# Kernel optimization log

Measured on AMD Instinct MI355X. Metric: run time of the kernel, lower is better.

Reference implementation:

```python
import jax, jax.numpy as jnp
import numpy as np

NUM_Q = 1000
DIM_S = 64
SIZE_M = 50
BATCH = 128
SEQ = 200


def setup_inputs() -> dict:
    key = jax.random.key(0)
    ks = jax.random.split(key, 16)
    s = 1.0 / np.sqrt(DIM_S)
    inp = {
        "q": jax.random.randint(ks[0], (BATCH, SEQ), 0, NUM_Q),
        "r": jax.random.randint(ks[1], (BATCH, SEQ), 0, 2),
        "at_s": jax.random.randint(ks[2], (BATCH, 16), 0, 30000),
        "at_m": jnp.ones((BATCH, 16), dtype=jnp.int64 if jax.config.jax_enable_x64 else jnp.int32),
        "k_emb": jax.random.normal(ks[3], (NUM_Q, DIM_S)) * s,
        "v_emb": jax.random.normal(ks[4], (2 * NUM_Q, DIM_S)) * s,
        "Mk": jax.random.normal(ks[5], (SIZE_M, DIM_S)) * s,
        "Mv0": jax.random.normal(ks[6], (SIZE_M, DIM_S)) * s,
        "We": jax.random.normal(ks[7], (DIM_S, DIM_S)) * s,
        "be": jnp.zeros((DIM_S,)),
        "Wa": jax.random.normal(ks[8], (DIM_S, DIM_S)) * s,
        "ba": jnp.zeros((DIM_S,)),
        "Wf": jax.random.normal(ks[9], (2 * DIM_S, DIM_S)) * s,
        "bf": jnp.zeros((DIM_S,)),
        "Wp": jax.random.normal(ks[10], (DIM_S, 1)) * s,
        "bp": jnp.zeros((1,)),
    }
    return inp


def reference(q, r, at_s, at_m, k_emb, v_emb, Mk, Mv0, We, be, Wa, ba, Wf, bf, Wp, bp):
    num_q = k_emb.shape[0]
    x = q + r * num_q                         # [B, n]
    k = k_emb[q]                              # [B, n, d]
    v = v_emb[x]                              # [B, n, d]
    w = jax.nn.softmax(jnp.einsum("bnd,md->bnm", k, Mk), axis=-1)  # [B, n, m]
    e = jax.nn.sigmoid(v @ We + be)           # erase gate [B, n, d]
    a = jnp.tanh(v @ Wa + ba)                 # add vector [B, n, d]

    B = q.shape[0]
    Mv_init = jnp.broadcast_to(Mv0[None], (B,) + Mv0.shape)  # [B, m, d]

    def step(Mvt, inp):
        et, at_, wt = inp                     # [B,d], [B,d], [B,m]
        Mvt = Mvt * (1.0 - wt[:, :, None] * et[:, None, :]) + wt[:, :, None] * at_[:, None, :]
        return Mvt, Mvt

    xs = (e.transpose(1, 0, 2), a.transpose(1, 0, 2), w.transpose(1, 0, 2))
    _, Mv_seq = jax.lax.scan(step, Mv_init, xs)             # [n, B, m, d]
    Mv = jnp.concatenate([Mv_init[None], Mv_seq], axis=0)   # [n+1, B, m, d]
    Mv = Mv.transpose(1, 0, 2, 3)                            # [B, n+1, m, d]

    read = jnp.einsum("bnm,bnmd->bnd", w, Mv[:, :-1])        # read from pre-update memory
    f = jnp.tanh(jnp.concatenate([read, k], axis=-1) @ Wf + bf)
    p = jax.nn.sigmoid((f @ Wp + bp)).squeeze(-1)            # [B, n]; dropout is identity at eval
    return p, Mv
```

## Files before the change

kernel.cpp:

```cpp
#include <hip/hip_runtime.h>
#include <hip/hip_bf16.h>

typedef __hip_bfloat16 bf16;

#define BATCH 128
#define SEQ   200
#define NUMQ  1000
#define DD    64
#define MM    50
#define CHUNKS 10
#define CLEN   20


__device__ __forceinline__ float rdlane(float v, int j) {
    return __uint_as_float(__builtin_amdgcn_readlane(__float_as_uint(v), j));
}

__global__ __launch_bounds__(256) void k1_precompute(
    const int* __restrict__ q, const int* __restrict__ r,
    const float* __restrict__ k_emb, const float* __restrict__ v_emb,
    const float* __restrict__ Mk,
    const float* __restrict__ We, const float* __restrict__ be,
    const float* __restrict__ Wa, const float* __restrict__ ba,
    float* __restrict__ w_buf, float* __restrict__ e_buf, float* __restrict__ a_buf)
{
    __shared__ float Mk_l[MM][DD + 1];
    __shared__ float kv_l[4][128];

    const int tid = threadIdx.x;
    for (int i = tid; i < MM * DD; i += 256)
        Mk_l[i >> 6][i & 63] = Mk[i];

    const int w    = tid >> 6;
    const int lane = tid & 63;
    const int row  = blockIdx.x * 4 + w;

    int qi = q[row], ri = r[row];
    qi = min(max(qi, 0), NUMQ - 1);
    ri = min(max(ri, 0), 1);
    const int xi = qi + ri * NUMQ;

    kv_l[w][lane]      = k_emb[(size_t)qi * DD + lane];
    kv_l[w][64 + lane] = v_emb[(size_t)xi * DD + lane];
    __syncthreads();

    float s = 0.f;
    if (lane < MM) {
        #pragma unroll
        for (int dd = 0; dd < DD; ++dd)
            s += kv_l[w][dd] * Mk_l[lane][dd];
    }
    float mx = (lane < MM) ? s : -1e30f;
    #pragma unroll
    for (int off = 32; off >= 1; off >>= 1)
        mx = fmaxf(mx, __shfl_xor(mx, off, 64));
    float ex = (lane < MM) ? expf(s - mx) : 0.f;
    float sm = ex;
    #pragma unroll
    for (int off = 32; off >= 1; off >>= 1)
        sm += __shfl_xor(sm, off, 64);
    if (lane < MM)
        w_buf[(size_t)row * MM + lane] = ex / sm;

    float ea = be[lane], aa = ba[lane];
    #pragma unroll
    for (int dd = 0; dd < DD; ++dd) {
        const float vb = kv_l[w][64 + dd];
        ea = __builtin_fmaf(vb, We[dd * DD + lane], ea);
        aa = __builtin_fmaf(vb, Wa[dd * DD + lane], aa);
    }
    e_buf[(size_t)row * DD + lane] = 1.f / (1.f + expf(-ea));
    a_buf[(size_t)row * DD + lane] = tanhf(aa);
}

__global__ __launch_bounds__(64) void k2a_summary(
    const float* __restrict__ w_buf, const float* __restrict__ e_buf,
    const float* __restrict__ a_buf,
    float* __restrict__ Abuf, float* __restrict__ Bbuf)
{
    const int bid  = blockIdx.x;
    const int b    = bid / CHUNKS;
    const int c    = bid % CHUNKS;
    const int lane = threadIdx.x;
    const int t0   = c * CLEN;

    const float* wrow = w_buf + (size_t)b * SEQ * MM;
    const float* erow = e_buf + (size_t)b * SEQ * DD;
    const float* arow = a_buf + (size_t)b * SEQ * DD;

    float A[MM], B[MM];
    #pragma unroll
    for (int j = 0; j < MM; ++j) { A[j] = 1.f; B[j] = 0.f; }

    float wreg = (lane < MM) ? wrow[(size_t)t0 * MM + lane] : 0.f;
    float e_n  = erow[(size_t)t0 * DD + lane];
    float a_n  = arow[(size_t)t0 * DD + lane];

    for (int tt = 0; tt < CLEN; ++tt) {
        const int t = t0 + tt;
        const float e_v = e_n, a_v = a_n, wcur = wreg;
        if (t + 1 < SEQ) {
            wreg = (lane < MM) ? wrow[(size_t)(t + 1) * MM + lane] : 0.f;
            e_n  = erow[(size_t)(t + 1) * DD + lane];
            a_n  = arow[(size_t)(t + 1) * DD + lane];
        }
        #pragma unroll
        for (int j = 0; j < MM; ++j) {
            const float wj = rdlane(wcur, j);
            const float f  = __builtin_fmaf(-wj, e_v, 1.f);
            const float g  = wj * a_v;
            A[j] *= f;
            B[j] = __builtin_fmaf(B[j], f, g);
        }
    }

    float* Ao = Abuf + ((size_t)bid * MM) * DD;
    float* Bo = Bbuf + ((size_t)bid * MM) * DD;
    #pragma unroll
    for (int j = 0; j < MM; ++j) {
        Ao[j * DD + lane] = A[j];
        Bo[j * DD + lane] = B[j];
    }
}

__global__ __launch_bounds__(64) void k2c_replay(
    const float* __restrict__ Mv0,
    const float* __restrict__ w_buf, const float* __restrict__ e_buf,
    const float* __restrict__ a_buf,
    const float* __restrict__ Abuf, const float* __restrict__ Bbuf,
    float* __restrict__ read_buf, float* __restrict__ out_Mv)
{
    const int bid  = blockIdx.x;
    const int b    = bid / CHUNKS;
    const int c    = bid % CHUNKS;
    const int lane = threadIdx.x;
    const int t0   = c * CLEN;

    float Mv[MM];
    float* outb = out_Mv + (size_t)b * (SEQ + 1) * MM * DD;
    #pragma unroll
    for (int j = 0; j < MM; ++j)
        Mv[j] = Mv0[j * DD + lane];
    if (c == 0) {
        #pragma unroll
        for (int j = 0; j < MM; ++j)
            outb[j * DD + lane] = Mv[j];
    }

    for (int cc = 0; cc < c; ++cc) {
        const float* Ao = Abuf + ((size_t)(b * CHUNKS + cc) * MM) * DD;
        const float* Bo = Bbuf + ((size_t)(b * CHUNKS + cc) * MM) * DD;
        #pragma unroll
        for (int j = 0; j < MM; ++j)
            Mv[j] = __builtin_fmaf(Ao[j * DD + lane], Mv[j], Bo[j * DD + lane]);
    }

    const float* wrow = w_buf + (size_t)b * SEQ * MM;
    const float* erow = e_buf + (size_t)b * SEQ * DD;
    const float* arow = a_buf + (size_t)b * SEQ * DD;
    float*       rrow = read_buf + (size_t)b * SEQ * DD;

    float wreg = (lane < MM) ? wrow[(size_t)t0 * MM + lane] : 0.f;
    float e_n  = erow[(size_t)t0 * DD + lane];
    float a_n  = arow[(size_t)t0 * DD + lane];

    for (int tt = 0; tt < CLEN; ++tt) {
        const int t = t0 + tt;
        const float e_v = e_n, a_v = a_n, wcur = wreg;
        if (t + 1 < SEQ) {
            wreg = (lane < MM) ? wrow[(size_t)(t + 1) * MM + lane] : 0.f;
            e_n  = erow[(size_t)(t + 1) * DD + lane];
            a_n  = arow[(size_t)(t + 1) * DD + lane];
        }
        float* outt = outb + (size_t)(t + 1) * MM * DD;
        float racc0 = 0.f, racc1 = 0.f;
        #pragma unroll
        for (int j = 0; j < MM; ++j) {
            const float wj    = rdlane(wcur, j);
            const float m_old = Mv[j];
            if (j & 1) racc1 = __builtin_fmaf(wj, m_old, racc1);
            else       racc0 = __builtin_fmaf(wj, m_old, racc0);
            Mv[j] = __builtin_fmaf(wj, __builtin_fmaf(-e_v, m_old, a_v), m_old);
            outt[j * DD + lane] = Mv[j];
        }
        rrow[(size_t)t * DD + lane] = racc0 + racc1;
    }
}

__global__ __launch_bounds__(64) void k2_scan_chunked(
    const float* __restrict__ Mv0,
    const float* __restrict__ w_buf, const float* __restrict__ e_buf,
    const float* __restrict__ a_buf,
    float* __restrict__ read_buf, float* __restrict__ out_Mv)
{
    const int bid  = blockIdx.x;
    const int b    = bid / CHUNKS;
    const int c    = bid % CHUNKS;
    const int lane = threadIdx.x;
    const int t0   = c * CLEN;

    float Mv[MM];
    float* outb = out_Mv + (size_t)b * (SEQ + 1) * MM * DD;
    #pragma unroll
    for (int j = 0; j < MM; ++j)
        Mv[j] = Mv0[j * DD + lane];
    if (c == 0) {
        #pragma unroll
        for (int j = 0; j < MM; ++j)
            outb[j * DD + lane] = Mv[j];
    }

    const float* wrow = w_buf + (size_t)b * SEQ * MM;
    const float* erow = e_buf + (size_t)b * SEQ * DD;
    const float* arow = a_buf + (size_t)b * SEQ * DD;
    float*       rrow = read_buf + (size_t)b * SEQ * DD;

    float wreg = (lane < MM) ? wrow[lane] : 0.f;
    float e_n  = erow[lane];
    float a_n  = arow[lane];

    for (int t = 0; t < t0; ++t) {
        const float e_v = e_n, a_v = a_n, wcur = wreg;
        wreg = (lane < MM) ? wrow[(size_t)(t + 1) * MM + lane] : 0.f;
        e_n  = erow[(size_t)(t + 1) * DD + lane];
        a_n  = arow[(size_t)(t + 1) * DD + lane];
        #pragma unroll
        for (int j = 0; j < MM; ++j) {
            const float wj = rdlane(wcur, j);
            Mv[j] = __builtin_fmaf(wj, __builtin_fmaf(-e_v, Mv[j], a_v), Mv[j]);
        }
    }

    for (int tt = 0; tt < CLEN; ++tt) {
        const int t = t0 + tt;
        const float e_v = e_n, a_v = a_n, wcur = wreg;
        if (t + 1 < SEQ) {
            wreg = (lane < MM) ? wrow[(size_t)(t + 1) * MM + lane] : 0.f;
            e_n  = erow[(size_t)(t + 1) * DD + lane];
            a_n  = arow[(size_t)(t + 1) * DD + lane];
        }
        float* outt = outb + (size_t)(t + 1) * MM * DD;
        float racc0 = 0.f, racc1 = 0.f;
        #pragma unroll
        for (int j = 0; j < MM; ++j) {
            const float wj    = rdlane(wcur, j);
            const float m_old = Mv[j];
            if (j & 1) racc1 = __builtin_fmaf(wj, m_old, racc1);
            else       racc0 = __builtin_fmaf(wj, m_old, racc0);
            Mv[j] = __builtin_fmaf(wj, __builtin_fmaf(-e_v, m_old, a_v), m_old);
            outt[j * DD + lane] = Mv[j];
        }
        rrow[(size_t)t * DD + lane] = racc0 + racc1;
    }
}

__global__ __launch_bounds__(256) void k3_out(
    const int* __restrict__ q,
    const float* __restrict__ k_emb,
    const float* __restrict__ read_buf,
    const float* __restrict__ Wf, const float* __restrict__ bfb,
    const float* __restrict__ Wp, const float* __restrict__ bp,
    float* __restrict__ out_p)
{
    __shared__ float rk[4][128];
    const int tid  = threadIdx.x;
    const int w    = tid >> 6;
    const int lane = tid & 63;
    const int row  = blockIdx.x * 4 + w;

    int qi = q[row];
    qi = min(max(qi, 0), NUMQ - 1);
    rk[w][lane]      = read_buf[(size_t)row * DD + lane];
    rk[w][64 + lane] = k_emb[(size_t)qi * DD + lane];
    __syncthreads();

    float acc = bfb[lane];
    #pragma unroll
    for (int i = 0; i < 2 * DD; ++i)
        acc = __builtin_fmaf(rk[w][i], Wf[i * DD + lane], acc);
    const float f = tanhf(acc);

    float pv = f * Wp[lane];
    #pragma unroll
    for (int off = 32; off >= 1; off >>= 1)
        pv += __shfl_xor(pv, off, 64);

    if (lane == 0)
        out_p[row] = 1.f / (1.f + expf(-(pv + bp[0])));
}

__global__ __launch_bounds__(640) void dkvmn_fused(
    const int* q_, const int* r_,
    const float* k_emb, const float* v_emb, const float* Mk, const float* Mv0,
    const float* We, const float* be, const float* Wa, const float* ba,
    const float* Wf, const float* bfb, const float* Wp, const float* bp,
    float* out_p, float* out_Mv)
{
    __shared__ float Mk_l[MM][DD + 1];
    __shared__ bf16  ring[SEQ][DD];
    __shared__ int   q_row[SEQ], x_row[SEQ];
    __shared__ float kbuf[DD], vbuf[DD], vbuf2[DD];
    __shared__ float wst[MM], est[DD], ast[DD];
    __shared__ float partial[640];
    __shared__ float bias_e[DD], bias_a[DD];

    const int b    = blockIdx.x;
    const int tid  = threadIdx.x;
    const int wv   = tid >> 6;
    const int lane = tid & 63;

    for (int t = tid; t < SEQ; t += 640) {
        int qi = q_[b * SEQ + t], ri = r_[b * SEQ + t];
        qi = min(max(qi, 0), NUMQ - 1); ri = min(max(ri, 0), 1);
        q_row[t] = qi; x_row[t] = qi + ri * NUMQ;
    }
    for (int i = tid; i < MM * DD; i += 640) Mk_l[i >> 6][i & 63] = Mk[i];
    if (tid < DD) { bias_e[tid] = be[tid]; bias_a[tid] = ba[tid]; }

    const int d  = lane;
    const int m0 = wv * 5;
    float* outb = out_Mv + (size_t)b * (SEQ + 1) * MM * DD;
    float Mv[5];
    #pragma unroll
    for (int j = 0; j < 5; ++j) {
        Mv[j] = Mv0[(m0 + j) * DD + d];
        outb[(m0 + j) * DD + d] = Mv[j];
    }
    __syncthreads();

    float kf_n = 0.f, vf_n = 0.f, vf2_n = 0.f;
    if (wv == 0) kf_n  = k_emb[(size_t)q_row[0] * DD + lane];
    if (wv == 1) vf_n  = v_emb[(size_t)x_row[0] * DD + lane];
    if (wv == 2) vf2_n = v_emb[(size_t)x_row[0] * DD + lane];

    for (int t = 0; t < SEQ; ++t) {
        if (wv == 0) {
            kbuf[lane] = kf_n;
            if (t + 1 < SEQ) kf_n = k_emb[(size_t)q_row[t + 1] * DD + lane];
            float s = 0.f;
            if (lane < MM) {
                #pragma unroll
                for (int dd = 0; dd < DD; ++dd) s += kbuf[dd] * Mk_l[lane][dd];
            }
            float mx = (lane < MM) ? s : -1e30f;
            #pragma unroll
            for (int off = 32; off >= 1; off >>= 1) mx = fmaxf(mx, __shfl_xor(mx, off, 64));
            float ex = (lane < MM) ? expf(s - mx) : 0.f;
            float sm = ex;
            #pragma unroll
            for (int off = 32; off >= 1; off >>= 1) sm += __shfl_xor(sm, off, 64);
            if (lane < MM) wst[lane] = ex / sm;
        } else if (wv == 1) {
            vbuf[lane] = vf_n;
            if (t + 1 < SEQ) vf_n = v_emb[(size_t)x_row[t + 1] * DD + lane];
            float acc = bias_e[lane];
            #pragma unroll
            for (int dd = 0; dd < DD; ++dd) acc += vbuf[dd] * We[dd * DD + lane];
            est[lane] = 1.f / (1.f + expf(-acc));
        } else if (wv == 2) {
            vbuf2[lane] = vf2_n;
            if (t + 1 < SEQ) vf2_n = v_emb[(size_t)x_row[t + 1] * DD + lane];
            float acc = bias_a[lane];
            #pragma unroll
            for (int dd = 0; dd < DD; ++dd) acc += vbuf2[dd] * Wa[dd * DD + lane];
            ast[lane] = tanhf(acc);
        }
        __syncthreads();

        const float e_v = est[d];
        const float a_v = ast[d];
        float racc = 0.f;
        float* outt = outb + (size_t)(t + 1) * MM * DD;
        #pragma unroll
        for (int j = 0; j < 5; ++j) {
            const float wvv = wst[m0 + j];
            racc += wvv * Mv[j];
            Mv[j] = __builtin_fmaf(wvv, a_v - e_v * Mv[j], Mv[j]);
            outt[(m0 + j) * DD + d] = Mv[j];
        }
        partial[tid] = racc;
        __syncthreads();

        if (tid < DD) {
            float rr = 0.f;
            #pragma unroll
            for (int g = 0; g < 10; ++g) rr += partial[g * 64 + tid];
            ring[t][tid] = (bf16)rr;
        }
    }
    __syncthreads();

    for (int t = wv; t < SEQ; t += 10) {
        const int qi = q_row[t];
        const float kreg = k_emb[(size_t)qi * DD + lane];
        float acc = bfb[lane];
        #pragma unroll
        for (int i = 0; i < DD; ++i) acc += (float)ring[t][i] * Wf[i * DD + lane];
        #pragma unroll
        for (int i = 0; i < DD; ++i) acc += __shfl(kreg, i, 64) * Wf[(DD + i) * DD + lane];
        const float f = tanhf(acc);
        float pv = f * Wp[lane];
        #pragma unroll
        for (int off = 32; off >= 1; off >>= 1) pv += __shfl_xor(pv, off, 64);
        if (lane == 0)
            out_p[(size_t)b * SEQ + t] = 1.f / (1.f + expf(-(pv + bp[0])));
    }
}

extern "C" void kernel_launch(void* const* d_in, const int* in_sizes, int n_in,
                              void* d_out, int out_size, void* d_ws, size_t ws_size,
                              hipStream_t stream) {
    const int*   q     = (const int*)  d_in[0];
    const int*   r     = (const int*)  d_in[1];
    const float* k_emb = (const float*)d_in[4];
    const float* v_emb = (const float*)d_in[5];
    const float* Mk    = (const float*)d_in[6];
    const float* Mv0   = (const float*)d_in[7];
    const float* We    = (const float*)d_in[8];
    const float* be    = (const float*)d_in[9];
    const float* Wa    = (const float*)d_in[10];
    const float* ba    = (const float*)d_in[11];
    const float* Wf    = (const float*)d_in[12];
    const float* bfb   = (const float*)d_in[13];
    const float* Wp    = (const float*)d_in[14];
    const float* bp    = (const float*)d_in[15];

    float* out_p  = (float*)d_out;
    float* out_Mv = (float*)d_out + BATCH * SEQ;

    const size_t N_WEA  = (size_t)BATCH * SEQ * (MM + 3 * DD);
    const size_t N_SUM  = (size_t)BATCH * CHUNKS * MM * DD;
    const size_t WS_BASE = N_WEA * sizeof(float);
    const size_t WS_HIER = WS_BASE + 2 * N_SUM * sizeof(float);

    const int rows = BATCH * SEQ;

    if (ws_size >= WS_BASE) {
        float* w_buf    = (float*)d_ws;
        float* e_buf    = w_buf + (size_t)BATCH * SEQ * MM;
        float* a_buf    = e_buf + (size_t)BATCH * SEQ * DD;
        float* read_buf = a_buf + (size_t)BATCH * SEQ * DD;

        hipLaunchKernelGGL(k1_precompute, dim3(rows / 4), dim3(256), 0, stream,
                           q, r, k_emb, v_emb, Mk, We, be, Wa, ba, w_buf, e_buf, a_buf);

        if (ws_size >= WS_HIER) {
            float* Abuf = read_buf + (size_t)BATCH * SEQ * DD;
            float* Bbuf = Abuf + N_SUM;
            hipLaunchKernelGGL(k2a_summary, dim3(BATCH * CHUNKS), dim3(64), 0, stream,
                               w_buf, e_buf, a_buf, Abuf, Bbuf);
            hipLaunchKernelGGL(k2c_replay, dim3(BATCH * CHUNKS), dim3(64), 0, stream,
                               Mv0, w_buf, e_buf, a_buf, Abuf, Bbuf, read_buf, out_Mv);
        } else {
            hipLaunchKernelGGL(k2_scan_chunked, dim3(BATCH * CHUNKS), dim3(64), 0, stream,
                               Mv0, w_buf, e_buf, a_buf, read_buf, out_Mv);
        }

        hipLaunchKernelGGL(k3_out, dim3(rows / 4), dim3(256), 0, stream,
                           q, k_emb, read_buf, Wf, bfb, Wp, bp, out_p);
    } else {
        hipLaunchKernelGGL(dkvmn_fused, dim3(BATCH), dim3(640), 0, stream,
                           q, r, k_emb, v_emb, Mk, Mv0, We, be, Wa, ba,
                           Wf, bfb, Wp, bp, out_p, out_Mv);
    }
}
```

Baseline: 184.0 us.

## Fuse precompute into chunk summary and output head into replay kernel

```diff
diff --git a/kernel.cpp b/kernel.cpp
--- a/kernel.cpp
+++ b/kernel.cpp
@@ -15,6 +15,189 @@
 __device__ __forceinline__ float rdlane(float v, int j) {
     return __uint_as_float(__builtin_amdgcn_readlane(__float_as_uint(v), j));
 }
+
+
+__global__ __launch_bounds__(64) void k2a_fused(
+    const int* __restrict__ q, const int* __restrict__ r,
+    const float* __restrict__ k_emb, const float* __restrict__ v_emb,
+    const float* __restrict__ Mk,
+    const float* __restrict__ We, const float* __restrict__ be,
+    const float* __restrict__ Wa, const float* __restrict__ ba,
+    float* __restrict__ w_buf, float* __restrict__ e_buf, float* __restrict__ a_buf,
+    float* __restrict__ Abuf, float* __restrict__ Bbuf)
+{
+    __shared__ float Mk_l[MM][DD + 1];
+    __shared__ float krow[DD], vrow[DD];
+
+    const int bid  = blockIdx.x;
+    const int b    = bid / CHUNKS;
+    const int c    = bid % CHUNKS;
+    const int lane = threadIdx.x;
+    const int t0   = c * CLEN;
+
+    for (int i = lane; i < MM * DD; i += 64)
+        Mk_l[i >> 6][i & 63] = Mk[i];
+
+    float A[MM], B[MM];
+    #pragma unroll
+    for (int j = 0; j < MM; ++j) { A[j] = 1.f; B[j] = 0.f; }
+
+    const float be_l = be[lane];
+    const float ba_l = ba[lane];
+
+    for (int tt = 0; tt < CLEN; ++tt) {
+        const int t   = t0 + tt;
+        const int row = b * SEQ + t;
+        int qi = q[row], ri = r[row];
+        qi = min(max(qi, 0), NUMQ - 1);
+        ri = min(max(ri, 0), 1);
+        const int xi = qi + ri * NUMQ;
+
+        krow[lane] = k_emb[(size_t)qi * DD + lane];
+        vrow[lane] = v_emb[(size_t)xi * DD + lane];
+
+        float s = 0.f;
+        if (lane < MM) {
+            #pragma unroll
+            for (int dd = 0; dd < DD; ++dd)
+                s = __builtin_fmaf(krow[dd], Mk_l[lane][dd], s);
+        }
+        float mx = (lane < MM) ? s : -1e30f;
+        #pragma unroll
+        for (int off = 32; off >= 1; off >>= 1)
+            mx = fmaxf(mx, __shfl_xor(mx, off, 64));
+        float ex = (lane < MM) ? expf(s - mx) : 0.f;
+        float sm = ex;
+        #pragma unroll
+        for (int off = 32; off >= 1; off >>= 1)
+            sm += __shfl_xor(sm, off, 64);
+        const float wv_m = ex / sm;
+        if (lane < MM) w_buf[(size_t)row * MM + lane] = wv_m;
+
+        float ea = be_l, aa = ba_l;
+        #pragma unroll
+        for (int dd = 0; dd < DD; ++dd) {
+            const float vb = vrow[dd];
+            ea = __builtin_fmaf(vb, We[dd * DD + lane], ea);
+            aa = __builtin_fmaf(vb, Wa[dd * DD + lane], aa);
+        }
+        const float e_v = 1.f / (1.f + expf(-ea));
+        const float a_v = tanhf(aa);
+        e_buf[(size_t)row * DD + lane] = e_v;
+        a_buf[(size_t)row * DD + lane] = a_v;
+
+        #pragma unroll
+        for (int j = 0; j < MM; ++j) {
+            const float wj = rdlane(wv_m, j);
+            const float f  = __builtin_fmaf(-wj, e_v, 1.f);
+            A[j] *= f;
+            B[j] = __builtin_fmaf(B[j], f, wj * a_v);
+        }
+    }
+
+    float* Ao = Abuf + (size_t)bid * MM * DD;
+    float* Bo = Bbuf + (size_t)bid * MM * DD;
+    #pragma unroll
+    for (int j = 0; j < MM; ++j) {
+        Ao[j * DD + lane] = A[j];
+        Bo[j * DD + lane] = B[j];
+    }
+}
+
+__global__ __launch_bounds__(64) void k2c_fused(
+    const int* __restrict__ q,
+    const float* __restrict__ k_emb, const float* __restrict__ Mv0,
+    const float* __restrict__ w_buf, const float* __restrict__ e_buf,
+    const float* __restrict__ a_buf,
+    const float* __restrict__ Abuf, const float* __restrict__ Bbuf,
+    const float* __restrict__ Wf, const float* __restrict__ bfb,
+    const float* __restrict__ Wp, const float* __restrict__ bp,
+    float* __restrict__ out_p, float* __restrict__ out_Mv)
+{
+    __shared__ float rbuf[DD], kbuf[DD];
+
+    const int bid  = blockIdx.x;
+    const int b    = bid / CHUNKS;
+    const int c    = bid % CHUNKS;
+    const int lane = threadIdx.x;
+    const int t0   = c * CLEN;
+
+    float Mv[MM];
+    float* outb = out_Mv + (size_t)b * (SEQ + 1) * MM * DD;
+    #pragma unroll
+    for (int j = 0; j < MM; ++j)
+        Mv[j] = Mv0[j * DD + lane];
+    if (c == 0) {
+        #pragma unroll
+        for (int j = 0; j < MM; ++j)
+            __builtin_nontemporal_store(Mv[j], &outb[j * DD + lane]);
+    }
+
+    for (int cc = 0; cc < c; ++cc) {
+        const float* Ao = Abuf + (size_t)(b * CHUNKS + cc) * MM * DD;
+        const float* Bo = Bbuf + (size_t)(b * CHUNKS + cc) * MM * DD;
+        #pragma unroll
+        for (int j = 0; j < MM; ++j)
+            Mv[j] = __builtin_fmaf(Ao[j * DD + lane], Mv[j], Bo[j * DD + lane]);
+    }
+
+    const float* wrow = w_buf + (size_t)b * SEQ * MM;
+    const float* erow = e_buf + (size_t)b * SEQ * DD;
+    const float* arow = a_buf + (size_t)b * SEQ * DD;
+
+    const float bf_l = bfb[lane];
+    const float wp_l = Wp[lane];
+    const float bp0  = bp[0];
+
+    float wreg = (lane < MM) ? wrow[(size_t)t0 * MM + lane] : 0.f;
+    float e_n  = erow[(size_t)t0 * DD + lane];
+    float a_n  = arow[(size_t)t0 * DD + lane];
+    int   qin  = min(max(q[b * SEQ + t0], 0), NUMQ - 1);
+    float kk_n = k_emb[(size_t)qin * DD + lane];
+
+    for (int tt = 0; tt < CLEN; ++tt) {
+        const int t   = t0 + tt;
+        const int row = b * SEQ + t;
+        const float e_v = e_n, a_v = a_n, wcur = wreg, kk = kk_n;
+        if (t + 1 < SEQ) {
+            wreg = (lane < MM) ? wrow[(size_t)(t + 1) * MM + lane] : 0.f;
+            e_n  = erow[(size_t)(t + 1) * DD + lane];
+            a_n  = arow[(size_t)(t + 1) * DD + lane];
+            qin  = min(max(q[row + 1], 0), NUMQ - 1);
+            kk_n = k_emb[(size_t)qin * DD + lane];
+        }
+
+        float* outt = outb + (size_t)(t + 1) * MM * DD;
+        float racc0 = 0.f, racc1 = 0.f;
+        #pragma unroll
+        for (int j = 0; j < MM; ++j) {
+            const float wj    = rdlane(wcur, j);
+            const float m_old = Mv[j];
+            if (j & 1) racc1 = __builtin_fmaf(wj, m_old, racc1);
+            else       racc0 = __builtin_fmaf(wj, m_old, racc0);
+            Mv[j] = __builtin_fmaf(wj, __builtin_fmaf(-e_v, m_old, a_v), m_old);
+            __builtin_nontemporal_store(Mv[j], &outt[j * DD + lane]);
+        }
+
+        rbuf[lane] = racc0 + racc1;
+        kbuf[lane] = kk;
+        float acc = bf_l;
+        #pragma unroll
+        for (int i = 0; i < DD; ++i)
+            acc = __builtin_fmaf(rbuf[i], Wf[i * DD + lane], acc);
+        #pragma unroll
+        for (int i = 0; i < DD; ++i)
+            acc = __builtin_fmaf(kbuf[i], Wf[(DD + i) * DD + lane], acc);
+        const float f = tanhf(acc);
+        float pv = f * wp_l;
+        #pragma unroll
+        for (int off = 32; off >= 1; off >>= 1)
+            pv += __shfl_xor(pv, off, 64);
+        if (lane == 0)
+            out_p[row] = 1.f / (1.f + expf(-(pv + bp0)));
+    }
+}
+
 
 __global__ __launch_bounds__(256) void k1_precompute(
     const int* __restrict__ q, const int* __restrict__ r,
@@ -71,120 +254,6 @@
     }
     e_buf[(size_t)row * DD + lane] = 1.f / (1.f + expf(-ea));
     a_buf[(size_t)row * DD + lane] = tanhf(aa);
-}
-
-__global__ __launch_bounds__(64) void k2a_summary(
-    const float* __restrict__ w_buf, const float* __restrict__ e_buf,
-    const float* __restrict__ a_buf,
-    float* __restrict__ Abuf, float* __restrict__ Bbuf)
-{
-    const int bid  = blockIdx.x;
-    const int b    = bid / CHUNKS;
-    const int c    = bid % CHUNKS;
-    const int lane = threadIdx.x;
-    const int t0   = c * CLEN;
-
-    const float* wrow = w_buf + (size_t)b * SEQ * MM;
-    const float* erow = e_buf + (size_t)b * SEQ * DD;
-    const float* arow = a_buf + (size_t)b * SEQ * DD;
-
-    float A[MM], B[MM];
-    #pragma unroll
-    for (int j = 0; j < MM; ++j) { A[j] = 1.f; B[j] = 0.f; }
-
-    float wreg = (lane < MM) ? wrow[(size_t)t0 * MM + lane] : 0.f;
-    float e_n  = erow[(size_t)t0 * DD + lane];
-    float a_n  = arow[(size_t)t0 * DD + lane];
-
-    for (int tt = 0; tt < CLEN; ++tt) {
-        const int t = t0 + tt;
-        const float e_v = e_n, a_v = a_n, wcur = wreg;
-        if (t + 1 < SEQ) {
-            wreg = (lane < MM) ? wrow[(size_t)(t + 1) * MM + lane] : 0.f;
-            e_n  = erow[(size_t)(t + 1) * DD + lane];
-            a_n  = arow[(size_t)(t + 1) * DD + lane];
-        }
-        #pragma unroll
-        for (int j = 0; j < MM; ++j) {
-            const float wj = rdlane(wcur, j);
-            const float f  = __builtin_fmaf(-wj, e_v, 1.f);
-            const float g  = wj * a_v;
-            A[j] *= f;
-            B[j] = __builtin_fmaf(B[j], f, g);
-        }
-    }
-
-    float* Ao = Abuf + ((size_t)bid * MM) * DD;
-    float* Bo = Bbuf + ((size_t)bid * MM) * DD;
-    #pragma unroll
-    for (int j = 0; j < MM; ++j) {
-        Ao[j * DD + lane] = A[j];
-        Bo[j * DD + lane] = B[j];
-    }
-}
-
-__global__ __launch_bounds__(64) void k2c_replay(
-    const float* __restrict__ Mv0,
-    const float* __restrict__ w_buf, const float* __restrict__ e_buf,
-    const float* __restrict__ a_buf,
-    const float* __restrict__ Abuf, const float* __restrict__ Bbuf,
-    float* __restrict__ read_buf, float* __restrict__ out_Mv)
-{
-    const int bid  = blockIdx.x;
-    const int b    = bid / CHUNKS;
-    const int c    = bid % CHUNKS;
-    const int lane = threadIdx.x;
-    const int t0   = c * CLEN;
-
-    float Mv[MM];
-    float* outb = out_Mv + (size_t)b * (SEQ + 1) * MM * DD;
-    #pragma unroll
-    for (int j = 0; j < MM; ++j)
-        Mv[j] = Mv0[j * DD + lane];
-    if (c == 0) {
-        #pragma unroll
-        for (int j = 0; j < MM; ++j)
-            outb[j * DD + lane] = Mv[j];
-    }
-
-    for (int cc = 0; cc < c; ++cc) {
-        const float* Ao = Abuf + ((size_t)(b * CHUNKS + cc) * MM) * DD;
-        const float* Bo = Bbuf + ((size_t)(b * CHUNKS + cc) * MM) * DD;
-        #pragma unroll
-        for (int j = 0; j < MM; ++j)
-            Mv[j] = __builtin_fmaf(Ao[j * DD + lane], Mv[j], Bo[j * DD + lane]);
-    }
-
-    const float* wrow = w_buf + (size_t)b * SEQ * MM;
-    const float* erow = e_buf + (size_t)b * SEQ * DD;
-    const float* arow = a_buf + (size_t)b * SEQ * DD;
-    float*       rrow = read_buf + (size_t)b * SEQ * DD;
-
-    float wreg = (lane < MM) ? wrow[(size_t)t0 * MM + lane] : 0.f;
-    float e_n  = erow[(size_t)t0 * DD + lane];
-    float a_n  = arow[(size_t)t0 * DD + lane];
-
-    for (int tt = 0; tt < CLEN; ++tt) {
-        const int t = t0 + tt;
-        const float e_v = e_n, a_v = a_n, wcur = wreg;
-        if (t + 1 < SEQ) {
-            wreg = (lane < MM) ? wrow[(size_t)(t + 1) * MM + lane] : 0.f;
-            e_n  = erow[(size_t)(t + 1) * DD + lane];
-            a_n  = arow[(size_t)(t + 1) * DD + lane];
-        }
-        float* outt = outb + (size_t)(t + 1) * MM * DD;
-        float racc0 = 0.f, racc1 = 0.f;
-        #pragma unroll
-        for (int j = 0; j < MM; ++j) {
-            const float wj    = rdlane(wcur, j);
-            const float m_old = Mv[j];
-            if (j & 1) racc1 = __builtin_fmaf(wj, m_old, racc1);
-            else       racc0 = __builtin_fmaf(wj, m_old, racc0);
-            Mv[j] = __builtin_fmaf(wj, __builtin_fmaf(-e_v, m_old, a_v), m_old);
-            outt[j * DD + lane] = Mv[j];
-        }
-        rrow[(size_t)t * DD + lane] = racc0 + racc1;
-    }
 }
 
 __global__ __launch_bounds__(64) void k2_scan_chunked(
@@ -428,34 +497,37 @@
     float* out_p  = (float*)d_out;
     float* out_Mv = (float*)d_out + BATCH * SEQ;
 
-    const size_t N_WEA  = (size_t)BATCH * SEQ * (MM + 3 * DD);
+    const size_t N_W    = (size_t)BATCH * SEQ * MM;
+    const size_t N_D    = (size_t)BATCH * SEQ * DD;
     const size_t N_SUM  = (size_t)BATCH * CHUNKS * MM * DD;
-    const size_t WS_BASE = N_WEA * sizeof(float);
-    const size_t WS_HIER = WS_BASE + 2 * N_SUM * sizeof(float);
+    const size_t WS_NEW  = (N_W + 2 * N_D + 2 * N_SUM) * sizeof(float);
+    const size_t WS_CHNK = (N_W + 3 * N_D) * sizeof(float);
 
     const int rows = BATCH * SEQ;
 
-    if (ws_size >= WS_BASE) {
+    if (ws_size >= WS_NEW) {
+        float* w_buf = (float*)d_ws;
+        float* e_buf = w_buf + N_W;
+        float* a_buf = e_buf + N_D;
+        float* Abuf  = a_buf + N_D;
+        float* Bbuf  = Abuf + N_SUM;
+
+        hipLaunchKernelGGL(k2a_fused, dim3(BATCH * CHUNKS), dim3(64), 0, stream,
+                           q, r, k_emb, v_emb, Mk, We, be, Wa, ba,
+                           w_buf, e_buf, a_buf, Abuf, Bbuf);
+        hipLaunchKernelGGL(k2c_fused, dim3(BATCH * CHUNKS), dim3(64), 0, stream,
+                           q, k_emb, Mv0, w_buf, e_buf, a_buf, Abuf, Bbuf,
+                           Wf, bfb, Wp, bp, out_p, out_Mv);
+    } else if (ws_size >= WS_CHNK) {
         float* w_buf    = (float*)d_ws;
-        float* e_buf    = w_buf + (size_t)BATCH * SEQ * MM;
-        float* a_buf    = e_buf + (size_t)BATCH * SEQ * DD;
-        float* read_buf = a_buf + (size_t)BATCH * SEQ * DD;
+        float* e_buf    = w_buf + N_W;
+        float* a_buf    = e_buf + N_D;
+        float* read_buf = a_buf + N_D;
 
         hipLaunchKernelGGL(k1_precompute, dim3(rows / 4), dim3(256), 0, stream,
                            q, r, k_emb, v_emb, Mk, We, be, Wa, ba, w_buf, e_buf, a_buf);
-
-        if (ws_size >= WS_HIER) {
-            float* Abuf = read_buf + (size_t)BATCH * SEQ * DD;
-            float* Bbuf = Abuf + N_SUM;
-            hipLaunchKernelGGL(k2a_summary, dim3(BATCH * CHUNKS), dim3(64), 0, stream,
-                               w_buf, e_buf, a_buf, Abuf, Bbuf);
-            hipLaunchKernelGGL(k2c_replay, dim3(BATCH * CHUNKS), dim3(64), 0, stream,
-                               Mv0, w_buf, e_buf, a_buf, Abuf, Bbuf, read_buf, out_Mv);
-        } else {
-            hipLaunchKernelGGL(k2_scan_chunked, dim3(BATCH * CHUNKS), dim3(64), 0, stream,
-                               Mv0, w_buf, e_buf, a_buf, read_buf, out_Mv);
-        }
-
+        hipLaunchKernelGGL(k2_scan_chunked, dim3(BATCH * CHUNKS), dim3(64), 0, stream,
+                           Mv0, w_buf, e_buf, a_buf, read_buf, out_Mv);
         hipLaunchKernelGGL(k3_out, dim3(rows / 4), dim3(256), 0, stream,
                            q, k_emb, read_buf, Wf, bfb, Wp, bp, out_p);
     } else {
```

Measured after the change: 215.4 us. 17.0% more time.
